# Kernel optimization log

Hardware: AMD Instinct MI355X
Metric: run time of the kernel (lower is better)

## Reference

```python
import jax, jax.numpy as jnp
import numpy as np

GRID_DIMS = (64, 64, 64)
GRID_LOWER = np.array([0.0, 0.0, 0.0], np.float32)
GRID_STEPS = np.array([0.015625, 0.015625, 0.015625], np.float32)
RADIUS = 0.03125
STENCIL = 2  # ceil(radius / step)


def _poly6(d2, h):
    # standard SPH poly6 smoothing kernel: 315/(64 pi h^9) (h^2 - d^2)^3, d <= h
    c = np.float32(315.0 / (64.0 * np.pi * h ** 9))
    return jnp.where(d2 <= h * h, c * (h * h - d2) ** 3, 0.0)


def particles2grid(locs, data, density):
    # locs [B,N,3], data [B,N,C], density [B,N] -> grid [B,X,Y,Z,C]
    B, N, _ = locs.shape
    C = data.shape[-1]
    X, Y, Z = GRID_DIMS
    dims = jnp.array(GRID_DIMS, jnp.int32)
    r = jnp.arange(-STENCIL, STENCIL + 1)
    offs = jnp.stack(jnp.meshgrid(r, r, r, indexing='ij'), -1).reshape(-1, 3)  # [K,3]
    base = jnp.floor((locs - GRID_LOWER) / GRID_STEPS).astype(jnp.int32)        # [B,N,3]
    cells = base[:, :, None, :] + offs                                          # [B,N,K,3]
    centers = GRID_LOWER + (cells.astype(locs.dtype) + 0.5) * GRID_STEPS
    d2 = jnp.sum((centers - locs[:, :, None, :]) ** 2, -1)                      # [B,N,K]
    w = _poly6(d2, RADIUS)
    w = jnp.where(jnp.all((cells >= 0) & (cells < dims), -1), w, 0.0)
    contrib = w[..., None] * (data / density[..., None])[:, :, None, :]         # [B,N,K,C]
    cells = jnp.clip(cells, 0, dims - 1)
    flat = (cells[..., 0] * Y + cells[..., 1]) * Z + cells[..., 2]              # [B,N,K]

    def splat(f, c):
        return jnp.zeros((X * Y * Z, C), data.dtype).at[f.reshape(-1)].add(c.reshape(-1, C))

    return jax.vmap(splat)(flat, contrib).reshape(B, X, Y, Z, C)


def grid2particles(grid, locs):
    # trilinear interpolation of grid [B,X,Y,Z,C] at particle locations [B,N,3]
    B, X, Y, Z, C = grid.shape
    dims = jnp.array([X, Y, Z], jnp.int32)
    pos = (locs - GRID_LOWER) / GRID_STEPS - 0.5                                # cell-center coords
    i0 = jnp.floor(pos).astype(jnp.int32)
    frac = pos - i0.astype(locs.dtype)
    gflat = grid.reshape(B, X * Y * Z, C)
    gather = jax.vmap(lambda g, f: g[f])                                        # [B,N] -> [B,N,C]
    out = jnp.zeros((B, locs.shape[1], C), grid.dtype)
    for dx in (0, 1):
        for dy in (0, 1):
            for dz in (0, 1):
                off = jnp.array([dx, dy, dz], jnp.int32)
                idx = i0 + off
                wd = jnp.where(off == 1, frac, 1.0 - frac)                      # [B,N,3]
                w = wd[..., 0] * wd[..., 1] * wd[..., 2]
                w = jnp.where(jnp.all((idx >= 0) & (idx < dims), -1), w, 0.0)
                idx = jnp.clip(idx, 0, dims - 1)
                flat = (idx[..., 0] * Y + idx[..., 1]) * Z + idx[..., 2]
                out = out + w[..., None] * gather(gflat, flat)
    return out


def conv3d(x, w, b):
    y = jax.lax.conv_general_dilated(x, w, (1, 1, 1), 'SAME',
                                     dimension_numbers=('NCDHW', 'OIDHW', 'NCDHW'))
    return y + b[None, :, None, None, None]


def prelu(x, a):
    return jnp.where(x >= 0, x, a * x)


def setup_inputs() -> dict:
    key = jax.random.key(0)
    ks = jax.random.split(key, 8)
    B, N = 2, 32768
    Cin, K, Cout = 4, 32, 4
    s = lambda fan: np.float32(1.0 / np.sqrt(fan * 27))
    return {
        'locs': jax.random.uniform(ks[0], (B, N, 3), jnp.float32),
        'data': jax.random.normal(ks[1], (B, N, Cin), jnp.float32),
        'density': jax.random.uniform(ks[2], (B, N), jnp.float32, 0.5, 1.5),
        'W0': jax.random.normal(ks[3], (K, Cin, 3, 3, 3), jnp.float32) * s(Cin),
        'b0': jnp.zeros((K,), jnp.float32),
        'W1': jax.random.normal(ks[4], (K, K, 3, 3, 3), jnp.float32) * s(K),
        'b1': jnp.zeros((K,), jnp.float32),
        'W2': jax.random.normal(ks[5], (K, K, 3, 3, 3), jnp.float32) * s(K),
        'b2': jnp.zeros((K,), jnp.float32),
        'W3': jax.random.normal(ks[6], (Cout, K, 3, 3, 3), jnp.float32) * s(K),
        'b3': jnp.zeros((Cout,), jnp.float32),
        'a0': jnp.full((1,), 0.25, jnp.float32),
        'a1': jnp.full((1,), 0.25, jnp.float32),
        'a2': jnp.full((1,), 0.25, jnp.float32),
    }


def reference(locs, data, density, W0, b0, W1, b1, W2, b2, W3, b3, a0, a1, a2):
    grid = particles2grid(locs, data, density)            # [B,X,Y,Z,Cin]
    g = jnp.transpose(grid, (0, 4, 1, 2, 3))              # NCDHW
    g = prelu(conv3d(g, W0, b0), a0)
    g = prelu(conv3d(g, W1, b1), a1)
    g = prelu(conv3d(g, W2, b2), a2)
    g = conv3d(g, W3, b3)
    g = jnp.transpose(g, (0, 2, 3, 4, 1))                 # [B,X,Y,Z,Cout]
    return grid2particles(g, locs)                        # [B,N,Cout]
```

## Files before the change

### kernel.cpp

```cpp
#include <hip/hip_runtime.h>

#define BATCH 2
#define NPART 32768
#define GD 64
#define NVOX (BATCH * GD * GD * GD)

typedef unsigned short ushortT;
typedef __attribute__((ext_vector_type(8))) short short8;
typedef __attribute__((ext_vector_type(16))) float float16;

__device__ __forceinline__ float poly6_c() {
    const double H9 = 1.0 / 35184372088832.0;
    return (float)(315.0 / (64.0 * 3.14159265358979323846 * H9));
}

__device__ __forceinline__ ushortT bf16_rne(float f) {
    unsigned int u = __float_as_uint(f);
    u = (u + 0x7fffu + ((u >> 16) & 1u)) >> 16;
    return (ushortT)u;
}

__device__ __forceinline__ int imax(int a, int b) { return a > b ? a : b; }
__device__ __forceinline__ int imin(int a, int b) { return a < b ? a : b; }

__device__ __forceinline__ void load_lds16(const void* g, void* l) {
    __builtin_amdgcn_global_load_lds(
        (const __attribute__((address_space(1))) void*)g,
        (__attribute__((address_space(3))) void*)l, 16, 0, 0);
}

__global__ __launch_bounds__(256) void prep_kernel(
    int* __restrict__ zp,
    const float* __restrict__ W0, const float* __restrict__ W1,
    const float* __restrict__ W2, const float* __restrict__ W3,
    short* __restrict__ Bp) {
    int bid = blockIdx.x, tid = threadIdx.x;
    if (bid < 513) {
        int t = bid * 256 + tid;
        if (t < 131088) zp[t] = 0;
        return;
    }
    int t = (bid - 513) * 256 + tid;
    if (t >= 176 * 512) return;
    int kt = t >> 9;
    int l = (t >> 3) & 63, j = t & 7;
    int n = l & 31, q = l >> 5;
    float v = 0.f;
    if (kt < 14) {
        int k = kt * 16 + 8 * q + j;
        int tap = k >> 3, ic = k & 7;
        if (tap < 27 && ic < 4) v = W0[(n * 4 + ic) * 27 + tap];
    } else {
        const float* W; int O, s;
        if (kt < 68)       { W = W1; O = 32; s = kt - 14; }
        else if (kt < 122) { W = W2; O = 32; s = kt - 68; }
        else               { W = W3; O = 4;  s = kt - 122; }
        int h = s / 27, ss = s - h * 27;
        int gI = ss / 3, dy = ss - gI * 3;
        int dx = gI / 3, dz = gI - dx * 3;
        int tap = dx * 9 + dy * 3 + dz;
        int ic = h * 16 + q * 8 + j;
        if (n < O) v = W[(n * 32 + ic) * 27 + tap];
    }
    Bp[t] = (short)bf16_rne(v);
}

__global__ __launch_bounds__(256) void bin_count_kernel(
    const float* __restrict__ locs, int* __restrict__ counts) {
    int t = blockIdx.x * blockDim.x + threadIdx.x;
    if (t >= BATCH * NPART) return;
    int b = t >> 15;
    int bx = ((int)floorf(locs[t * 3 + 0] * 64.0f)) >> 1;
    int by = ((int)floorf(locs[t * 3 + 1] * 64.0f)) >> 1;
    int bz = ((int)floorf(locs[t * 3 + 2] * 64.0f)) >> 1;
    atomicAdd(&counts[b * 32768 + ((bx * 32) + by) * 32 + bz], 1);
}

__global__ __launch_bounds__(256) void scanA_kernel(
    const int* __restrict__ counts, int* __restrict__ offsets,
    int* __restrict__ blockSum) {
    __shared__ int sh[256];
    int tid = threadIdx.x, g = blockIdx.x;
    int v = counts[g * 256 + tid];
    sh[tid] = v;
    __syncthreads();
    for (int off = 1; off < 256; off <<= 1) {
        int u = (tid >= off) ? sh[tid - off] : 0;
        __syncthreads();
        sh[tid] += u;
        __syncthreads();
    }
    offsets[g * 256 + tid] = sh[tid] - v;
    if (tid == 255) blockSum[g] = sh[255];
}

__global__ __launch_bounds__(256) void scanB_kernel(
    int* __restrict__ offsets, const int* __restrict__ blockSum) {
    __shared__ int sh[256];
    int tid = threadIdx.x, g = blockIdx.x;
    sh[tid] = (tid < g) ? blockSum[tid] : 0;
    __syncthreads();
    for (int off = 128; off > 0; off >>= 1) {
        if (tid < off) sh[tid] += sh[tid + off];
        __syncthreads();
    }
    offsets[g * 256 + tid] += sh[0];
    if (g == 255 && tid == 255) offsets[65536] = BATCH * NPART;
}

__global__ __launch_bounds__(256) void bin_scatter_kernel(
    const float* __restrict__ locs, const float* __restrict__ data,
    const float* __restrict__ density, const int* __restrict__ offsets,
    int* __restrict__ cursor, float* __restrict__ payload) {
    int t = blockIdx.x * blockDim.x + threadIdx.x;
    if (t >= BATCH * NPART) return;
    int b = t >> 15;
    float px = locs[t * 3 + 0];
    float py = locs[t * 3 + 1];
    float pz = locs[t * 3 + 2];
    int bx = ((int)floorf(px * 64.0f)) >> 1;
    int by = ((int)floorf(py * 64.0f)) >> 1;
    int bz = ((int)floorf(pz * 64.0f)) >> 1;
    int bb = b * 32768 + ((bx * 32) + by) * 32 + bz;
    int slot = atomicAdd(&cursor[bb], 1);
    int idx = offsets[bb] + slot;
    float inv_d = 1.0f / density[t];
    float4 p0 = {px, py, pz, data[t * 4 + 0] * inv_d};
    float4 p1 = {data[t * 4 + 1] * inv_d, data[t * 4 + 2] * inv_d,
                 data[t * 4 + 3] * inv_d, 0.f};
    *(float4*)(payload + idx * 8)     = p0;
    *(float4*)(payload + idx * 8 + 4) = p1;
}

__global__ __launch_bounds__(256) void splat_gather_kernel(
    const float* __restrict__ payload, const int* __restrict__ offsets,
    ushortT* __restrict__ g8) {
    __shared__ float plist[256 * 8];
    __shared__ int segS[36];
    __shared__ int segP[37];
    __shared__ int shTot[1];

    int wg = blockIdx.x;
    int sb = wg & 511, b = wg >> 9;
    int X0 = (sb >> 6) * 8, Y0 = ((sb >> 3) & 7) * 8, Z0 = (sb & 7) * 8;
    int tid = threadIdx.x;

    int bxlo = imax(0, (X0 - 2) >> 1), bxhi = imin(31, (X0 + 9) >> 1);
    int bylo = imax(0, (Y0 - 2) >> 1), byhi = imin(31, (Y0 + 9) >> 1);
    int bzlo = imax(0, (Z0 - 2) >> 1), bzhi = imin(31, (Z0 + 9) >> 1);
    int ny = byhi - bylo + 1;
    int ns = (bxhi - bxlo + 1) * ny;
    if (tid < ns) {
        int bx = bxlo + tid / ny, by = bylo + tid % ny;
        int row = b * 32768 + (bx * 32 + by) * 32;
        int s = offsets[row + bzlo];
        int e = offsets[row + bzhi + 1];
        segS[tid] = s;
        segP[tid] = e - s;
    }
    __syncthreads();
    if (tid == 0) {
        int p = 0;
        for (int k = 0; k < ns; ++k) { int len = segP[k]; segP[k] = p; p += len; }
        segP[ns] = p;
        shTot[0] = p;
    }
    __syncthreads();

    const float step = 0.015625f;
    const float h2 = 0.03125f * 0.03125f;
    const float cc = poly6_c();
    int total = shTot[0];

    int l = tid & 63, w = tid >> 6;
    int cx = X0 + 4 * (w >> 1) + (l >> 4);
    int cy = Y0 + 4 * (w & 1) + ((l >> 2) & 3);
    int cz0 = Z0 + (l & 3);
    float xc  = ((float)cx  + 0.5f) * step;
    float yc  = ((float)cy  + 0.5f) * step;
    float zc0 = ((float)cz0 + 0.5f) * step;
    float zc1 = zc0 + 4.0f * step;

    float a00 = 0.f, a01 = 0.f, a02 = 0.f, a03 = 0.f;
    float a10 = 0.f, a11 = 0.f, a12 = 0.f, a13 = 0.f;

    int nchunks = (total + 255) >> 8;
    for (int ch = 0; ch < nchunks; ++ch) {
        __syncthreads();
        int jj = (ch << 8) + tid;
        if (jj < total) {
            int k = 0;
            while (jj >= segP[k + 1]) ++k;
            int idx = segS[k] + (jj - segP[k]);
            *(float4*)(plist + tid * 8)     = *(const float4*)(payload + idx * 8);
            *(float4*)(plist + tid * 8 + 4) = *(const float4*)(payload + idx * 8 + 4);
        }
        __syncthreads();
        int cnt = imin(256, total - (ch << 8));
        for (int p = 0; p < cnt; ++p) {
            float4 pa = *(const float4*)(plist + p * 8);
            float dx = pa.x - xc, dy = pa.y - yc;
            float dxy2 = fmaf(dy, dy, dx * dx);
            if (!__any(dxy2 <= h2)) continue;
            float4 pv = *(const float4*)(plist + p * 8 + 4);
            float dz0 = pa.z - zc0;
            float d20 = fmaf(dz0, dz0, dxy2);
            float u0 = fmaxf(h2 - d20, 0.f);
            float w0 = (cc * u0) * (u0 * u0);
            a00 = fmaf(w0, pa.w, a00);
            a01 = fmaf(w0, pv.x, a01);
            a02 = fmaf(w0, pv.y, a02);
            a03 = fmaf(w0, pv.z, a03);
            float dz1 = pa.z - zc1;
            float d21 = fmaf(dz1, dz1, dxy2);
            float u1 = fmaxf(h2 - d21, 0.f);
            float w1 = (cc * u1) * (u1 * u1);
            a10 = fmaf(w1, pa.w, a10);
            a11 = fmaf(w1, pv.x, a11);
            a12 = fmaf(w1, pv.y, a12);
            a13 = fmaf(w1, pv.z, a13);
        }
    }

    size_t cellBase = (size_t)(((b * 64 + cx) * 64 + cy) * 64);
    short8 o;
    o[0] = (short)bf16_rne(a00); o[1] = (short)bf16_rne(a01);
    o[2] = (short)bf16_rne(a02); o[3] = (short)bf16_rne(a03);
    o[4] = 0; o[5] = 0; o[6] = 0; o[7] = 0;
    *(short8*)(g8 + (cellBase + cz0) * 8) = o;
    o[0] = (short)bf16_rne(a10); o[1] = (short)bf16_rne(a11);
    o[2] = (short)bf16_rne(a12); o[3] = (short)bf16_rne(a13);
    *(short8*)(g8 + (cellBase + cz0 + 4) * 8) = o;
}

template <int ICG, int KT, bool FINAL>
__global__ __launch_bounds__(256, 3) void mfma_conv_kernel(
    const ushortT* __restrict__ in, const short* __restrict__ Bpack,
    const float* __restrict__ bias, const float* __restrict__ alpha,
    const float* __restrict__ zguard, void* __restrict__ outv) {
    constexpr int CIN  = ICG * 8;
    constexpr int PH   = (ICG == 1) ? 1 : 2;
    constexpr int NCHP = (ICG == 1) ? (24 * 34) : (24 * 2 * 34);
    constexpr int BUFS = NCHP * 8;
    __shared__ short lds[2 * BUFS];

    int wg = ((blockIdx.x & 7) << 7) | (blockIdx.x >> 3);
    int yq = wg & 15, xp = (wg >> 4) & 31, b = wg >> 9;
    int X0 = xp * 2, Y0 = yq * 4;
    int tid = threadIdx.x;
    const ushortT* inb = in + (size_t)b * (64 * 64 * 64 * CIN);

    int l = tid & 63, w = tid >> 6;
    int wx = w >> 1, wy2 = (w & 1) * 2;
    int n = l & 31, q = l >> 5;
    int laneZ = (l & 31) * 8;
    const short* bp = Bpack + (size_t)l * 8;
    float bval = FINAL ? (n < 4 ? bias[n] : 0.f) : bias[n];

    auto stage = [&](int ph) {
        int t = ph / PH, h = ph - t * PH;
        int zb = t * 32;
        short* dst = lds + (ph & 1) * BUFS;
#pragma unroll
        for (int it = 0; it < (NCHP + 255) / 256; ++it) {
            int ccid = it * 256 + tid;
            if (ccid < NCHP) {
                int col, icg2, zi;
                if constexpr (ICG == 1) {
                    col = ccid / 34; zi = ccid - col * 34; icg2 = 0;
                } else {
                    col = ccid / 68;
                    int rem = ccid - col * 68;
                    icg2 = rem / 34; zi = rem - icg2 * 34;
                }
                int gx = X0 + col / 6 - 1;
                int gy = Y0 + col % 6 - 1;
                int gz = zb + zi - 1;
                const void* src = (const void*)zguard;
                if ((unsigned)gx < 64u && (unsigned)gy < 64u && (unsigned)gz < 64u)
                    src = (const void*)(inb +
                        ((size_t)(((gx * 64) + gy) * 64 + gz)) * CIN + (h * 2 + icg2) * 8);
                load_lds16(src, (void*)(dst + ccid * 8));
            }
        }
    };

    stage(0);

#pragma unroll
    for (int tile = 0; tile < 2; ++tile) {
        int Z0 = tile * 32;
        float16 acc0, acc1;
#pragma unroll
        for (int r = 0; r < 16; ++r) { acc0[r] = bval; acc1[r] = bval; }

#pragma unroll
        for (int h = 0; h < PH; ++h) {
            int ph = tile * PH + h;
            __syncthreads();
            if (ph + 1 < 2 * PH) stage(ph + 1);
            const short* lb = lds + (ph & 1) * BUFS;

            if constexpr (ICG == 1) {
                short8 bf[4];
#pragma unroll
                for (int i = 0; i < 4; ++i) bf[i] = *(const short8*)(bp + i * 512);
#pragma unroll
                for (int kt = 0; kt < KT; ++kt) {
                    short8 bcur = bf[kt & 3];
                    if (kt + 4 < KT) bf[kt & 3] = *(const short8*)(bp + (kt + 4) * 512);
                    int tap0 = kt * 2, tap1 = kt * 2 + 1;
                    if (tap1 > 26) tap1 = 26;
                    int dx0 = tap0 / 9, r0 = tap0 - dx0 * 9, dy0 = r0 / 3, dz0 = r0 - dy0 * 3;
                    int dx1 = tap1 / 9, r1 = tap1 - dx1 * 9, dy1 = r1 / 3, dz1 = r1 - dy1 * 3;
#define AOFS1(c) (q ? ((((wx + dx1) * 6 + ((c) + dy1)) * 34 + dz1) * 8) \
                    : ((((wx + dx0) * 6 + ((c) + dy0)) * 34 + dz0) * 8))
                    short8 a0 = *(const short8*)(lb + AOFS1(wy2) + laneZ);
                    short8 a1 = *(const short8*)(lb + AOFS1(wy2 + 1) + laneZ);
#undef AOFS1
                    __builtin_amdgcn_s_setprio(1);
                    acc0 = __builtin_amdgcn_mfma_f32_32x32x16_bf16(a0, bcur, acc0, 0, 0, 0);
                    acc1 = __builtin_amdgcn_mfma_f32_32x32x16_bf16(a1, bcur, acc1, 0, 0, 0);
                    __builtin_amdgcn_s_setprio(0);
                }
            } else {
                short8 bf[4];
#pragma unroll
                for (int i = 0; i < 4; ++i)
                    bf[i] = *(const short8*)(bp + (h * 27 + i) * 512);
#pragma unroll
                for (int g = 0; g < 9; ++g) {
                    int dx = g / 3, dz = g - dx * 3;
                    short8 fr[4];
#pragma unroll
                    for (int k = 0; k < 4; ++k) {
                        int ofs = ((((wx + dx) * 6 + (wy2 + k)) * 2 + q) * 34 + dz) * 8;
                        fr[k] = *(const short8*)(lb + ofs + laneZ);
                    }
#pragma unroll
                    for (int dy = 0; dy < 3; ++dy) {
                        int k27 = g * 3 + dy;
                        short8 bcur = bf[k27 & 3];
                        if (k27 + 4 < 27)
                            bf[k27 & 3] = *(const short8*)(bp + (h * 27 + k27 + 4) * 512);
                        __builtin_amdgcn_s_setprio(1);
                        acc0 = __builtin_amdgcn_mfma_f32_32x32x16_bf16(fr[0 + dy], bcur, acc0, 0, 0, 0);
                        acc1 = __builtin_amdgcn_mfma_f32_32x32x16_bf16(fr[1 + dy], bcur, acc1, 0, 0, 0);
                        __builtin_amdgcn_s_setprio(0);
                    }
                }
            }
        }

        size_t base0 = (size_t)(((b * 64 + X0 + wx) * 64 + (Y0 + wy2)) * 64) + Z0;
        if constexpr (FINAL) {
            float* out = (float*)outv;
            if (n < 4) {
#pragma unroll
                for (int r = 0; r < 16; ++r) {
                    int z = (r & 3) + 8 * (r >> 2) + 4 * q;
                    out[(base0 + z) * 4 + n]      = acc0[r];
                    out[(base0 + 64 + z) * 4 + n] = acc1[r];
                }
            }
        } else {
            float a = alpha[0];
            ushortT* out = (ushortT*)outv;
#pragma unroll
            for (int r = 0; r < 16; ++r) {
                int z = (r & 3) + 8 * (r >> 2) + 4 * q;
                float v0 = acc0[r]; v0 = v0 >= 0.f ? v0 : a * v0;
                out[(base0 + z) * 32 + n] = bf16_rne(v0);
                float v1 = acc1[r]; v1 = v1 >= 0.f ? v1 : a * v1;
                out[(base0 + 64 + z) * 32 + n] = bf16_rne(v1);
            }
        }
    }
}

__global__ __launch_bounds__(256) void gather_kernel(
    const float* __restrict__ grid, const float* __restrict__ locs,
    float* __restrict__ out) {
    int t = blockIdx.x * blockDim.x + threadIdx.x;
    if (t >= BATCH * NPART) return;
    int b = t >> 15;

    float px = locs[t * 3 + 0] * 64.0f - 0.5f;
    float py = locs[t * 3 + 1] * 64.0f - 0.5f;
    float pz = locs[t * 3 + 2] * 64.0f - 0.5f;
    int ix = (int)floorf(px);
    int iy = (int)floorf(py);
    int iz = (int)floorf(pz);
    float fx = px - (float)ix;
    float fy = py - (float)iy;
    float fz = pz - (float)iz;

    const float* gb = grid + (size_t)b * GD * GD * GD * 4;
    float o0 = 0.f, o1 = 0.f, o2 = 0.f, o3 = 0.f;

#pragma unroll
    for (int dx = 0; dx < 2; ++dx) {
        int x = ix + dx;
        if ((unsigned)x > 63u) continue;
        float wx = dx ? fx : 1.0f - fx;
#pragma unroll
        for (int dy = 0; dy < 2; ++dy) {
            int y = iy + dy;
            if ((unsigned)y > 63u) continue;
            float wy = dy ? fy : 1.0f - fy;
#pragma unroll
            for (int dz = 0; dz < 2; ++dz) {
                int z = iz + dz;
                if ((unsigned)z > 63u) continue;
                float wz = dz ? fz : 1.0f - fz;
                float w = wx * wy * wz;
                const float4 g = *(const float4*)(gb + (size_t)(((x * GD) + y) * GD + z) * 4);
                o0 += w * g.x; o1 += w * g.y; o2 += w * g.z; o3 += w * g.w;
            }
        }
    }
    out[t * 4 + 0] = o0;
    out[t * 4 + 1] = o1;
    out[t * 4 + 2] = o2;
    out[t * 4 + 3] = o3;
}

extern "C" void kernel_launch(void* const* d_in, const int* in_sizes, int n_in,
                              void* d_out, int out_size, void* d_ws, size_t ws_size,
                              hipStream_t stream) {
    const float* locs    = (const float*)d_in[0];
    const float* data    = (const float*)d_in[1];
    const float* density = (const float*)d_in[2];
    const float* W0 = (const float*)d_in[3];
    const float* b0 = (const float*)d_in[4];
    const float* W1 = (const float*)d_in[5];
    const float* b1 = (const float*)d_in[6];
    const float* W2 = (const float*)d_in[7];
    const float* b2 = (const float*)d_in[8];
    const float* W3 = (const float*)d_in[9];
    const float* b3 = (const float*)d_in[10];
    const float* a0 = (const float*)d_in[11];
    const float* a1 = (const float*)d_in[12];
    const float* a2 = (const float*)d_in[13];
    float* out = (float*)d_out;

    char* ws = (char*)d_ws;
    ushortT* g8  = (ushortT*)(ws);
    ushortT* gA  = (ushortT*)(ws + 8388608);
    ushortT* gB  = (ushortT*)(ws + 41943040);
    float*  gF   = (float*)(ws + 75497472);
    short*  Bp   = (short*)(ws + 83886080);
    short*  Bp0  = Bp;
    short*  Bp1  = Bp + 14 * 512;
    short*  Bp2  = Bp + 68 * 512;
    short*  Bp3  = Bp + 122 * 512;
    float* zguard   = (float*)(ws + 84066240);
    int*   counts   = (int*)(ws + 84066304);
    int*   cursor   = (int*)(ws + 84328448);
    int*   offsets  = (int*)(ws + 84590592);
    int*   blockSum = (int*)(ws + 84852752);
    float* payload  = (float*)(ws + 84853888);

    prep_kernel<<<513 + 352, 256, 0, stream>>>((int*)zguard, W0, W1, W2, W3, Bp);

    bin_count_kernel<<<(BATCH * NPART) / 256, 256, 0, stream>>>(locs, counts);
    scanA_kernel<<<256, 256, 0, stream>>>(counts, offsets, blockSum);
    scanB_kernel<<<256, 256, 0, stream>>>(offsets, blockSum);
    bin_scatter_kernel<<<(BATCH * NPART) / 256, 256, 0, stream>>>(
        locs, data, density, offsets, cursor, payload);

    splat_gather_kernel<<<BATCH * 512, 256, 0, stream>>>(payload, offsets, g8);

    const int CGRID = 1024;
    mfma_conv_kernel< 1, 14, false><<<CGRID, 256, 0, stream>>>(g8, Bp0, b0, a0, zguard, gA);
    mfma_conv_kernel< 4, 54, false><<<CGRID, 256, 0, stream>>>(gA, Bp1, b1, a1, zguard, gB);
    mfma_conv_kernel< 4, 54, false><<<CGRID, 256, 0, stream>>>(gB, Bp2, b2, a2, zguard, gA);
    mfma_conv_kernel< 4, 54, true ><<<CGRID, 256, 0, stream>>>(gA, Bp3, b3, b3, zguard, gF);

    gather_kernel<<<(BATCH * NPART) / 256, 256, 0, stream>>>(gF, locs, out);
}
```

Baseline: 277.9 us.

## Stage conv weights in LDS and reorder channel-half/z-tile loop

The MFMA conv kernel now copies each channel half's weight slab into shared memory once per block, instead of having every lane stream B fragments from global memory. For multi-group inputs the loop order becomes channel half outer and z tile inner, so each weight slab is loaded only once; this keeps four accumulator tiles live at the same time. The extra shared memory and registers lower the launch-bounds occupancy target from 3 to 2 blocks, and the s_setprio hints are removed. Extra barriers now separate the input-tile double buffering from the weight reload.

```diff
diff --git a/kernel.cpp b/kernel.cpp
--- a/kernel.cpp
+++ b/kernel.cpp
@@ -234,15 +234,16 @@
 }
 
 template <int ICG, int KT, bool FINAL>
-__global__ __launch_bounds__(256, 3) void mfma_conv_kernel(
+__global__ __launch_bounds__(256, 2) void mfma_conv_kernel(
     const ushortT* __restrict__ in, const short* __restrict__ Bpack,
     const float* __restrict__ bias, const float* __restrict__ alpha,
     const float* __restrict__ zguard, void* __restrict__ outv) {
     constexpr int CIN  = ICG * 8;
-    constexpr int PH   = (ICG == 1) ? 1 : 2;
     constexpr int NCHP = (ICG == 1) ? (24 * 34) : (24 * 2 * 34);
-    constexpr int BUFS = NCHP * 8;
-    __shared__ short lds[2 * BUFS];
+    constexpr int ABUF = NCHP * 8;
+    constexpr int BKT  = (ICG == 1) ? KT : 27;
+    constexpr int BBUF = BKT * 512;
+    __shared__ short lds[2 * ABUF + BBUF];
 
     int wg = ((blockIdx.x & 7) << 7) | (blockIdx.x >> 3);
     int yq = wg & 15, xp = (wg >> 4) & 31, b = wg >> 9;
@@ -254,13 +255,14 @@
     int wx = w >> 1, wy2 = (w & 1) * 2;
     int n = l & 31, q = l >> 5;
     int laneZ = (l & 31) * 8;
-    const short* bp = Bpack + (size_t)l * 8;
     float bval = FINAL ? (n < 4 ? bias[n] : 0.f) : bias[n];
-
-    auto stage = [&](int ph) {
-        int t = ph / PH, h = ph - t * PH;
+    const short* Bl = lds + 2 * ABUF;
+
+    auto stageA = [&](int p) {
+        int h, t;
+        if constexpr (ICG == 1) { h = 0; t = p; } else { h = p >> 1; t = p & 1; }
         int zb = t * 32;
-        short* dst = lds + (ph & 1) * BUFS;
+        short* dst = lds + (p & 1) * ABUF;
 #pragma unroll
         for (int it = 0; it < (NCHP + 255) / 256; ++it) {
             int ccid = it * 256 + tid;
@@ -285,73 +287,58 @@
         }
     };
 
-    stage(0);
-
-#pragma unroll
-    for (int tile = 0; tile < 2; ++tile) {
-        int Z0 = tile * 32;
-        float16 acc0, acc1;
-#pragma unroll
-        for (int r = 0; r < 16; ++r) { acc0[r] = bval; acc1[r] = bval; }
-
-#pragma unroll
-        for (int h = 0; h < PH; ++h) {
-            int ph = tile * PH + h;
-            __syncthreads();
-            if (ph + 1 < 2 * PH) stage(ph + 1);
-            const short* lb = lds + (ph & 1) * BUFS;
-
-            if constexpr (ICG == 1) {
-                short8 bf[4];
-#pragma unroll
-                for (int i = 0; i < 4; ++i) bf[i] = *(const short8*)(bp + i * 512);
-#pragma unroll
-                for (int kt = 0; kt < KT; ++kt) {
-                    short8 bcur = bf[kt & 3];
-                    if (kt + 4 < KT) bf[kt & 3] = *(const short8*)(bp + (kt + 4) * 512);
-                    int tap0 = kt * 2, tap1 = kt * 2 + 1;
-                    if (tap1 > 26) tap1 = 26;
-                    int dx0 = tap0 / 9, r0 = tap0 - dx0 * 9, dy0 = r0 / 3, dz0 = r0 - dy0 * 3;
-                    int dx1 = tap1 / 9, r1 = tap1 - dx1 * 9, dy1 = r1 / 3, dz1 = r1 - dy1 * 3;
+    auto loadB = [&](int h) {
+        const short* src0 = Bpack + (size_t)h * BBUF;
+        short* dst = lds + 2 * ABUF;
+        constexpr int NB = BBUF / 8;
+#pragma unroll
+        for (int it = 0; it < (NB + 255) / 256; ++it) {
+            int ccid = it * 256 + tid;
+            if (ccid < NB)
+                load_lds16((const void*)(src0 + ccid * 8), (void*)(dst + ccid * 8));
+        }
+    };
+
+    auto computeP = [&](int p, float16& c0, float16& c1) {
+        const short* lb = lds + (p & 1) * ABUF;
+        if constexpr (ICG == 1) {
+#pragma unroll
+            for (int kt = 0; kt < KT; ++kt) {
+                short8 bcur = *(const short8*)(Bl + kt * 512 + l * 8);
+                int tap0 = kt * 2, tap1 = kt * 2 + 1;
+                if (tap1 > 26) tap1 = 26;
+                int dx0 = tap0 / 9, r0 = tap0 - dx0 * 9, dy0 = r0 / 3, dz0 = r0 - dy0 * 3;
+                int dx1 = tap1 / 9, r1 = tap1 - dx1 * 9, dy1 = r1 / 3, dz1 = r1 - dy1 * 3;
 #define AOFS1(c) (q ? ((((wx + dx1) * 6 + ((c) + dy1)) * 34 + dz1) * 8) \
                     : ((((wx + dx0) * 6 + ((c) + dy0)) * 34 + dz0) * 8))
-                    short8 a0 = *(const short8*)(lb + AOFS1(wy2) + laneZ);
-                    short8 a1 = *(const short8*)(lb + AOFS1(wy2 + 1) + laneZ);
+                short8 a0 = *(const short8*)(lb + AOFS1(wy2) + laneZ);
+                short8 a1 = *(const short8*)(lb + AOFS1(wy2 + 1) + laneZ);
 #undef AOFS1
-                    __builtin_amdgcn_s_setprio(1);
-                    acc0 = __builtin_amdgcn_mfma_f32_32x32x16_bf16(a0, bcur, acc0, 0, 0, 0);
-                    acc1 = __builtin_amdgcn_mfma_f32_32x32x16_bf16(a1, bcur, acc1, 0, 0, 0);
-                    __builtin_amdgcn_s_setprio(0);
+                c0 = __builtin_amdgcn_mfma_f32_32x32x16_bf16(a0, bcur, c0, 0, 0, 0);
+                c1 = __builtin_amdgcn_mfma_f32_32x32x16_bf16(a1, bcur, c1, 0, 0, 0);
+            }
+        } else {
+#pragma unroll
+            for (int g = 0; g < 9; ++g) {
+                int dx = g / 3, dz = g - dx * 3;
+                short8 fr[4];
+#pragma unroll
+                for (int k = 0; k < 4; ++k) {
+                    int ofs = ((((wx + dx) * 6 + (wy2 + k)) * 2 + q) * 34 + dz) * 8;
+                    fr[k] = *(const short8*)(lb + ofs + laneZ);
                 }
-            } else {
-                short8 bf[4];
-#pragma unroll
-                for (int i = 0; i < 4; ++i)
-                    bf[i] = *(const short8*)(bp + (h * 27 + i) * 512);
-#pragma unroll
-                for (int g = 0; g < 9; ++g) {
-                    int dx = g / 3, dz = g - dx * 3;
-                    short8 fr[4];
-#pragma unroll
-                    for (int k = 0; k < 4; ++k) {
-                        int ofs = ((((wx + dx) * 6 + (wy2 + k)) * 2 + q) * 34 + dz) * 8;
-                        fr[k] = *(const short8*)(lb + ofs + laneZ);
-                    }
-#pragma unroll
-                    for (int dy = 0; dy < 3; ++dy) {
-                        int k27 = g * 3 + dy;
-                        short8 bcur = bf[k27 & 3];
-                        if (k27 + 4 < 27)
-                            bf[k27 & 3] = *(const short8*)(bp + (h * 27 + k27 + 4) * 512);
-                        __builtin_amdgcn_s_setprio(1);
-                        acc0 = __builtin_amdgcn_mfma_f32_32x32x16_bf16(fr[0 + dy], bcur, acc0, 0, 0, 0);
-                        acc1 = __builtin_amdgcn_mfma_f32_32x32x16_bf16(fr[1 + dy], bcur, acc1, 0, 0, 0);
-                        __builtin_amdgcn_s_setprio(0);
-                    }
+#pragma unroll
+                for (int dy = 0; dy < 3; ++dy) {
+                    short8 bcur = *(const short8*)(Bl + (g * 3 + dy) * 512 + l * 8);
+                    c0 = __builtin_amdgcn_mfma_f32_32x32x16_bf16(fr[0 + dy], bcur, c0, 0, 0, 0);
+                    c1 = __builtin_amdgcn_mfma_f32_32x32x16_bf16(fr[1 + dy], bcur, c1, 0, 0, 0);
                 }
             }
         }
-
+    };
+
+    auto epi = [&](int t, const float16& c0, const float16& c1) {
+        int Z0 = t * 32;
         size_t base0 = (size_t)(((b * 64 + X0 + wx) * 64 + (Y0 + wy2)) * 64) + Z0;
         if constexpr (FINAL) {
             float* out = (float*)outv;
@@ -359,8 +346,8 @@
 #pragma unroll
                 for (int r = 0; r < 16; ++r) {
                     int z = (r & 3) + 8 * (r >> 2) + 4 * q;
-                    out[(base0 + z) * 4 + n]      = acc0[r];
-                    out[(base0 + 64 + z) * 4 + n] = acc1[r];
+                    out[(base0 + z) * 4 + n]      = c0[r];
+                    out[(base0 + 64 + z) * 4 + n] = c1[r];
                 }
             }
         } else {
@@ -369,12 +356,47 @@
 #pragma unroll
             for (int r = 0; r < 16; ++r) {
                 int z = (r & 3) + 8 * (r >> 2) + 4 * q;
-                float v0 = acc0[r]; v0 = v0 >= 0.f ? v0 : a * v0;
+                float v0 = c0[r]; v0 = v0 >= 0.f ? v0 : a * v0;
                 out[(base0 + z) * 32 + n] = bf16_rne(v0);
-                float v1 = acc1[r]; v1 = v1 >= 0.f ? v1 : a * v1;
+                float v1 = c1[r]; v1 = v1 >= 0.f ? v1 : a * v1;
                 out[(base0 + 64 + z) * 32 + n] = bf16_rne(v1);
             }
         }
+    };
+
+    float16 a00, a01, a10, a11;
+#pragma unroll
+    for (int r = 0; r < 16; ++r) {
+        a00[r] = bval; a01[r] = bval; a10[r] = bval; a11[r] = bval;
+    }
+
+    stageA(0);
+    loadB(0);
+
+    if constexpr (ICG == 1) {
+        __syncthreads();
+        stageA(1);
+        computeP(0, a00, a01);
+        epi(0, a00, a01);
+        __syncthreads();
+        computeP(1, a10, a11);
+        epi(1, a10, a11);
+    } else {
+        __syncthreads();
+        stageA(1);
+        computeP(0, a00, a01);
+        __syncthreads();
+        stageA(2);
+        computeP(1, a10, a11);
+        __syncthreads();
+        loadB(1);
+        __syncthreads();
+        stageA(3);
+        computeP(2, a00, a01);
+        epi(0, a00, a01);
+        __syncthreads();
+        computeP(3, a10, a11);
+        epi(1, a10, a11);
     }
 }
 
```

New measurement: 239.8 us. 1.16x faster.
